# Performance work log

Hardware: AMD Instinct MI355X
Metric: run time of the kernel (lower is better)

## Reference

```python
import jax, jax.numpy as jnp
import numpy as np

EMB = 1024
HID = 2048
HEADS = 16
CONV = 4


def causal_conv1d(z, w):
    # z: [B, H, T], w: [H, K] depthwise causal conv
    K = w.shape[1]
    T = z.shape[-1]
    zp = jnp.pad(z, ((0, 0), (0, 0), (K - 1, 0)))  # [B, H, T+K-1]
    out = jnp.zeros_like(z)
    for k in range(K):  # tiny fixed loop over taps (K<=4)
        out = out + w[None, :, k, None] * jax.lax.dynamic_slice_in_dim(zp, k, T, axis=2)
    return out


def linear_scan(a, b):
    # h_t = a_t * h_{t-1} + b_t along last axis; associative scan
    def combine(c1, c2):
        a1, b1 = c1
        a2, b2 = c2
        return a1 * a2, a2 * b1 + b2
    _, h = jax.lax.associative_scan(combine, (a, b), axis=-1)
    return h


def setup_inputs() -> dict:
    key = jax.random.key(0)
    k1, k2, k3, k4 = jax.random.split(key, 4)
    x = jax.random.normal(k1, (4, 2048, EMB), dtype=jnp.float32)
    w1 = jax.random.normal(k2, (3 * HID, EMB), dtype=jnp.float32) * (EMB ** -0.5)
    w2 = jax.random.normal(k3, (EMB, HID), dtype=jnp.float32) * (HID ** -0.5)
    conv_weight = jax.random.normal(k4, (HID, CONV), dtype=jnp.float32) * (CONV ** -0.5)
    return {"x": x, "w1": w1, "w2": w2, "conv_weight": conv_weight}


def reference(x, w1, w2, conv_weight):
    bsz, seq_len, _ = x.shape
    head_dim = HID // HEADS
    y = jnp.einsum("bse,he->bsh", x, w1)  # [B, S, 3*HID]
    out1, z, h = jnp.split(y, 3, axis=-1)
    z = jnp.swapaxes(z, 1, 2)  # [B, HID, S]
    h = jnp.swapaxes(h, 1, 2)
    z = causal_conv1d(z, conv_weight)
    z = jax.nn.sigmoid(z)
    z = z.reshape(bsz * HEADS, head_dim, seq_len)
    h = h.reshape(bsz * HEADS, head_dim, seq_len)
    h = linear_scan(1.0 - z, z * h)
    out2 = jnp.swapaxes(h.reshape(bsz, HID, seq_len), 1, 2)  # [B, S, HID]
    out = jax.nn.silu(out1) * out2
    return jnp.einsum("bsh,eh->bse", out, w2)
```

## Files before the change

### kernel.cpp

```cpp
#include <hip/hip_runtime.h>
#include <cstdint>

#define EMB 1024
#define HID 2048
#define BATCH 4
#define SEQ 2048
#define MROWS (BATCH * SEQ)
#define N1 (3 * HID)
#define K1 EMB
#define N2 EMB
#define K2 HID

#define NX (MROWS * EMB)
#define NW1 (N1 * K1)
#define NW2 (N2 * K2)

#define SEG 64
#define SLEN (SEQ / SEG)

typedef unsigned short ushort_t;
typedef __bf16 bf16x8 __attribute__((ext_vector_type(8)));
typedef float f32x4 __attribute__((ext_vector_type(4)));
typedef ushort_t us4 __attribute__((ext_vector_type(4)));

__device__ __forceinline__ ushort_t f2bf(float f) {
    uint32_t u = __builtin_bit_cast(uint32_t, f);
    u += 0x7fffu + ((u >> 16) & 1u);
    return (ushort_t)(u >> 16);
}
__device__ __forceinline__ float bf2f(ushort_t h) {
    uint32_t u = ((uint32_t)h) << 16;
    return __builtin_bit_cast(float, u);
}
__device__ __forceinline__ float bflo(uint32_t v) {
    return __builtin_bit_cast(float, v << 16);
}
__device__ __forceinline__ float bfhi(uint32_t v) {
    return __builtin_bit_cast(float, v & 0xffff0000u);
}
__device__ __forceinline__ float sigm(float x) {
    return 1.f / (1.f + __expf(-x));
}

__device__ __forceinline__ void gload_lds16(const ushort_t* g, const ushort_t* l) {
    __builtin_amdgcn_global_load_lds(
        (const __attribute__((address_space(1))) void*)(uintptr_t)(g),
        (__attribute__((address_space(3))) void*)(uint32_t)(uintptr_t)(l),
        16, 0, 0);
}

__global__ __launch_bounds__(256) void cvt_kernel(
    const float* __restrict__ x, const float* __restrict__ w1,
    const float* __restrict__ w2, ushort_t* __restrict__ xb,
    ushort_t* __restrict__ w1b, ushort_t* __restrict__ w2b) {
    const int i = (blockIdx.x * 256 + threadIdx.x) * 4;
    const float* s;
    ushort_t* d;
    if (i < NX) {
        s = x + i; d = xb + i;
    } else if (i < NX + NW1) {
        s = w1 + (i - NX); d = w1b + (i - NX);
    } else {
        s = w2 + (i - NX - NW1); d = w2b + (i - NX - NW1);
    }
    const float4 v = *(const float4*)s;
    us4 o;
    o.x = f2bf(v.x); o.y = f2bf(v.y); o.z = f2bf(v.z); o.w = f2bf(v.w);
    *(us4*)d = o;
}

template <bool OUT_BF16>
__global__ __launch_bounds__(512, 2) void gemm256(
    const ushort_t* __restrict__ A, const ushort_t* __restrict__ B,
    void* __restrict__ Cv, int M, int N, int K) {
    __shared__ __align__(16) ushort_t sA[4][2][4096];
    __shared__ __align__(16) ushort_t sB[4][2][4096];

    const int tid  = threadIdx.x;
    const int lane = tid & 63;
    const int wave = tid >> 6;
    const int wm   = wave >> 2;
    const int wn   = wave & 3;
    const int quad = lane >> 4;
    const int l15  = lane & 15;

    int wg = blockIdx.x;
    const int nwg = gridDim.x;
    if ((nwg & 7) == 0) wg = (wg & 7) * (nwg >> 3) + (wg >> 3);
    const int nbx = N >> 8;
    const int bx = wg % nbx;
    const int by = wg / nbx;
    const long tm0 = (long)by << 8;
    const long tn0 = (long)bx << 8;

    const ushort_t* gA = A + (size_t)tm0 * K;
    const ushort_t* gB = B + (size_t)tn0 * K;

    const int l8g = lane >> 3;
    const int l7g = lane & 7;
    const int s8  = l7g ^ l8g;
    const int mloc = (l8g << 1) + (s8 >> 2);
    const uint32_t soff = (uint32_t)(wave * 16 + mloc) * (uint32_t)K +
                          (uint32_t)((s8 & 3) << 3);

    const auto STG = [&](int tt) {
        const int ib = tt & 3;
        const size_t ko = (size_t)tt * 32;
        gload_lds16(gA + ko + soff, &sA[ib][0][wave << 9]);
        gload_lds16(gA + ko + (size_t)128 * K + soff, &sA[ib][1][wave << 9]);
        gload_lds16(gB + ko + soff, &sB[ib][0][wave << 9]);
        gload_lds16(gB + ko + (size_t)128 * K + soff, &sB[ib][1][wave << 9]);
    };

    const int stored = ((((l15 & 1) << 2) + quad) ^ ((l15 >> 1) & 7));
    const int abase  = (l15 >> 1) * 64 + stored * 8;
    const int bbase  = ((wn & 1) << 11) + abase;

    f32x4 acc[8][4] = {};
    bf16x8 aX[8], bX[4], aY[8], bY[4];

    const int NT = K >> 5;

    STG(0); STG(1); STG(2);
    asm volatile("s_waitcnt vmcnt(4)" ::: "memory");
    __builtin_amdgcn_s_barrier();

    {
        const ushort_t* pa = &sA[0][wm][0];
        const ushort_t* pb = &sB[0][wn >> 1][0];
#pragma unroll
        for (int i = 0; i < 8; ++i) aX[i] = *(const bf16x8*)&pa[abase + i * 512];
#pragma unroll
        for (int j = 0; j < 4; ++j) bX[j] = *(const bf16x8*)&pb[bbase + j * 512];
    }

    const auto body = [&](int T, bf16x8 (&ac)[8], bf16x8 (&bc)[4],
                                 bf16x8 (&an)[8], bf16x8 (&bn)[4]) {
        const int ibn = (T + 1) & 3;
        const ushort_t* pa = &sA[ibn][wm][0];
        const ushort_t* pb = &sB[ibn][wn >> 1][0];
        const bool rd = (T + 1 < NT);
        const bool st = (T + 3 < NT);
        if (rd) {
#pragma unroll
            for (int i = 0; i < 4; ++i)
                an[i] = *(const bf16x8*)&pa[abase + i * 512];
        }
        __builtin_amdgcn_s_setprio(1);
#pragma unroll
        for (int i = 0; i < 4; ++i)
#pragma unroll
            for (int j = 0; j < 4; ++j)
                acc[i][j] = __builtin_amdgcn_mfma_f32_16x16x32_bf16(
                    ac[i], bc[j], acc[i][j], 0, 0, 0);
        __builtin_amdgcn_s_setprio(0);
        if (rd) {
#pragma unroll
            for (int i = 4; i < 8; ++i)
                an[i] = *(const bf16x8*)&pa[abase + i * 512];
#pragma unroll
            for (int j = 0; j < 4; ++j)
                bn[j] = *(const bf16x8*)&pb[bbase + j * 512];
        }
        __builtin_amdgcn_s_setprio(1);
#pragma unroll
        for (int i = 4; i < 8; ++i)
#pragma unroll
            for (int j = 0; j < 4; ++j)
                acc[i][j] = __builtin_amdgcn_mfma_f32_16x16x32_bf16(
                    ac[i], bc[j], acc[i][j], 0, 0, 0);
        __builtin_amdgcn_s_setprio(0);
        if (st) {
            STG(T + 3);
            asm volatile("s_waitcnt vmcnt(4)" ::: "memory");
        } else {
            asm volatile("s_waitcnt vmcnt(0)" ::: "memory");
        }
        __builtin_amdgcn_s_barrier();
    };

    for (int T = 0; T < NT; T += 2) {
        body(T, aX, bX, aY, bY);
        body(T + 1, aY, bY, aX, bX);
    }

#pragma unroll
    for (int i = 0; i < 8; ++i) {
        const long row0 = tm0 + wm * 128 + i * 16 + quad * 4;
#pragma unroll
        for (int j = 0; j < 4; ++j) {
            const long col = tn0 + wn * 64 + j * 16 + l15;
#pragma unroll
            for (int r = 0; r < 4; ++r) {
                if constexpr (OUT_BF16) {
                    ((ushort_t*)Cv)[(size_t)(row0 + r) * N + col] = f2bf(acc[i][j][r]);
                } else {
                    ((float*)Cv)[(size_t)(row0 + r) * N + col] = acc[i][j][r];
                }
            }
        }
    }
}

__device__ __forceinline__ void lda4(bf16x8 (&af)[2][4], const ushort_t* c,
                                     int arow, int quad, int sw) {
#pragma unroll
    for (int s = 0; s < 2; ++s)
#pragma unroll
        for (int i = 0; i < 4; ++i)
            af[s][i] = *(const bf16x8*)&c[(arow + i * 16) * 64 +
                                          (((s * 4 + quad) ^ sw) << 3)];
}

__global__ __launch_bounds__(512, 1) void gemm_mn(
    const ushort_t* __restrict__ A, const ushort_t* __restrict__ B,
    float* __restrict__ C, int M, int N, int K) {
    __shared__ __align__(16) ushort_t sA[3][2][8192];
    __shared__ __align__(16) ushort_t sB[3][8192];

    const int tid  = threadIdx.x;
    const int lane = tid & 63;
    const int wave = tid >> 6;
    const int wm   = wave >> 1;
    const int wn   = wave & 1;
    const int quad = lane >> 4;
    const int l15  = lane & 15;
    const int sw   = lane & 7;

    int wg = blockIdx.x;
    const int nwg = gridDim.x;
    if ((nwg & 7) == 0) wg = (wg & 7) * (nwg >> 3) + (wg >> 3);
    const int nbx = N >> 7;
    const int bx = wg % nbx;
    const int by = wg / nbx;
    const long tm0 = (long)by << 8;
    const long tn0 = (long)bx << 7;

    const ushort_t* gA = A + (size_t)tm0 * K;
    const ushort_t* gB = B + (size_t)tn0 * K;

    const int l8 = lane >> 3;
    const int ss = (lane & 7) ^ l8;
    const uint32_t rA = (uint32_t)((wave & 3) * 16 + l8 + (wave >> 2) * 128);
    const uint32_t rB = (uint32_t)(wave * 16 + l8);
    const uint32_t offA0 = rA * (uint32_t)K + (uint32_t)ss * 8u;
    const uint32_t offA1 = offA0 + 8u * (uint32_t)K;
    const uint32_t offB0 = rB * (uint32_t)K + (uint32_t)ss * 8u;
    const uint32_t offB1 = offB0 + 8u * (uint32_t)K;

    const auto stA = [&](int tt, int q) {
        ushort_t* d = &sA[tt % 3][q][wave << 10];
        const size_t ko = (size_t)tt * 64 + (size_t)q * 64 * (size_t)K;
        gload_lds16(gA + ko + offA0, d);
        gload_lds16(gA + ko + offA1, d + 512);
    };
    const auto stB = [&](int tt) {
        ushort_t* d = &sB[tt % 3][wave << 10];
        const size_t ko = (size_t)tt * 64;
        gload_lds16(gB + ko + offB0, d);
        gload_lds16(gB + ko + offB1, d + 512);
    };

    const int cq   = wm & 1;
    const int arow = (wm >> 1) * 64 + l15;
    const int bcol = wn * 64 + l15;

    f32x4 acc[4][4] = {};
    bf16x8 af[2][4], bf[2][4];

    const int NT = K >> 6;

    stA(0, 0); stA(0, 1); stB(0);
    stA(1, 0); stA(1, 1); stB(1);
    asm volatile("s_waitcnt vmcnt(6)" ::: "memory");
    __builtin_amdgcn_s_barrier();

    for (int T = 0; T < NT; ++T) {
        const int cur = T % 3;
        const ushort_t* pa = &sA[cur][cq][0];
        const ushort_t* pb = &sB[cur][0];
        const bool st2 = (T + 2 < NT);

        lda4(af, pa, arow, quad, sw);
        lda4(bf, pb, bcol, quad, sw);
        if (st2) { stA(T + 2, 0); stA(T + 2, 1); stB(T + 2); }
        __builtin_amdgcn_s_setprio(1);
#pragma unroll
        for (int s = 0; s < 2; ++s)
#pragma unroll
            for (int i = 0; i < 4; ++i)
#pragma unroll
                for (int j = 0; j < 4; ++j)
                    acc[i][j] = __builtin_amdgcn_mfma_f32_16x16x32_bf16(
                        af[s][i], bf[s][j], acc[i][j], 0, 0, 0);
        __builtin_amdgcn_s_setprio(0);
        if (st2)                asm volatile("s_waitcnt vmcnt(6)" ::: "memory");
        else if (T + 1 < NT)    asm volatile("s_waitcnt vmcnt(0)" ::: "memory");
        __builtin_amdgcn_s_barrier();
    }

#pragma unroll
    for (int i = 0; i < 4; ++i) {
        const long row0 = tm0 + wm * 64 + i * 16 + quad * 4;
#pragma unroll
        for (int j = 0; j < 4; ++j) {
            const long col = tn0 + wn * 64 + j * 16 + l15;
#pragma unroll
            for (int r = 0; r < 4; ++r)
                C[(size_t)(row0 + r) * N + col] = acc[i][j][r];
        }
    }
}

__global__ __launch_bounds__(256) void scan_part1(
    const ushort_t* __restrict__ y, const float* __restrict__ cw,
    float* __restrict__ Ag, float* __restrict__ Bg) {
    const int gid = blockIdx.x * 256 + threadIdx.x;
    const int ch  = (gid & 1023) * 2;
    const int bs  = gid >> 10;
    const int b   = bs >> 6;
    const int seg = bs & 63;
    const int t0  = seg * SLEN;
    const size_t rowbase = (size_t)b * SEQ;
    const ushort_t* yz = y + 2048 + ch;
    const ushort_t* yh = y + 4096 + ch;

    float w[2][4];
#pragma unroll
    for (int c = 0; c < 2; ++c)
#pragma unroll
        for (int k = 0; k < 4; ++k) w[c][k] = cw[(ch + c) * 4 + k];

    auto ld2 = [&](const ushort_t* p, int t) -> uint32_t {
        return *(const uint32_t*)(p + (rowbase + (size_t)t) * 6144);
    };
    auto zpair = [&](int t, float* out) {
        if (t < 0) { out[0] = 0.f; out[1] = 0.f; }
        else { uint32_t v = ld2(yz, t); out[0] = bflo(v); out[1] = bfhi(v); }
    };

    float z1[2], z2[2], z3[2], A[2] = {1.f, 1.f}, Bv[2] = {0.f, 0.f};
    zpair(t0 - 1, z1); zpair(t0 - 2, z2); zpair(t0 - 3, z3);

#pragma unroll 8
    for (int t = t0; t < t0 + SLEN; ++t) {
        const uint32_t vz = ld2(yz, t);
        const uint32_t vh = ld2(yh, t);
        const float zr[2] = {bflo(vz), bfhi(vz)};
        const float hr[2] = {bflo(vh), bfhi(vh)};
#pragma unroll
        for (int c = 0; c < 2; ++c) {
            const float cv = w[c][0] * z3[c] + w[c][1] * z2[c] +
                             w[c][2] * z1[c] + w[c][3] * zr[c];
            const float s = sigm(cv);
            z3[c] = z2[c]; z2[c] = z1[c]; z1[c] = zr[c];
            const float a = 1.f - s;
            A[c] *= a;
            Bv[c] = a * Bv[c] + s * hr[c];
        }
    }
    const size_t idx = ((size_t)b * SEG + seg) * HID + ch;
    *(float2*)&Ag[idx] = make_float2(A[0], A[1]);
    *(float2*)&Bg[idx] = make_float2(Bv[0], Bv[1]);
}

__global__ __launch_bounds__(256) void scan_part2(
    const float* __restrict__ Ag, const float* __restrict__ Bg,
    float* __restrict__ Cr) {
    const int gid = blockIdx.x * 256 + threadIdx.x;
    const int b  = gid >> 11;
    const int ch = gid & 2047;
    float carry = 0.f;
#pragma unroll
    for (int s = 0; s < SEG; ++s) {
        const size_t idx = ((size_t)b * SEG + s) * HID + ch;
        Cr[idx] = carry;
        carry = Ag[idx] * carry + Bg[idx];
    }
}

__global__ __launch_bounds__(256) void scan_part3(
    const ushort_t* __restrict__ y, const float* __restrict__ cw,
    const float* __restrict__ Cr, ushort_t* __restrict__ u) {
    const int gid = blockIdx.x * 256 + threadIdx.x;
    const int ch  = (gid & 1023) * 2;
    const int bs  = gid >> 10;
    const int b   = bs >> 6;
    const int seg = bs & 63;
    const int t0  = seg * SLEN;
    const size_t rowbase = (size_t)b * SEQ;
    const ushort_t* yo = y + ch;
    const ushort_t* yz = y + 2048 + ch;
    const ushort_t* yh = y + 4096 + ch;

    float w[2][4];
#pragma unroll
    for (int c = 0; c < 2; ++c)
#pragma unroll
        for (int k = 0; k < 4; ++k) w[c][k] = cw[(ch + c) * 4 + k];

    auto ld2 = [&](const ushort_t* p, int t) -> uint32_t {
        return *(const uint32_t*)(p + (rowbase + (size_t)t) * 6144);
    };
    auto zpair = [&](int t, float* out) {
        if (t < 0) { out[0] = 0.f; out[1] = 0.f; }
        else { uint32_t v = ld2(yz, t); out[0] = bflo(v); out[1] = bfhi(v); }
    };

    const size_t cidx = ((size_t)b * SEG + seg) * HID + ch;
    float h[2] = {Cr[cidx], Cr[cidx + 1]};
    float z1[2], z2[2], z3[2];
    zpair(t0 - 1, z1); zpair(t0 - 2, z2); zpair(t0 - 3, z3);

#pragma unroll 8
    for (int t = t0; t < t0 + SLEN; ++t) {
        const uint32_t vz = ld2(yz, t);
        const uint32_t vh = ld2(yh, t);
        const uint32_t vo = ld2(yo, t);
        const float zr[2] = {bflo(vz), bfhi(vz)};
        const float hr[2] = {bflo(vh), bfhi(vh)};
        const float o1[2] = {bflo(vo), bfhi(vo)};
        ushort_t res[2];
#pragma unroll
        for (int c = 0; c < 2; ++c) {
            const float cv = w[c][0] * z3[c] + w[c][1] * z2[c] +
                             w[c][2] * z1[c] + w[c][3] * zr[c];
            const float s = sigm(cv);
            z3[c] = z2[c]; z2[c] = z1[c]; z1[c] = zr[c];
            h[c] = (1.f - s) * h[c] + s * hr[c];
            const float sil = o1[c] * sigm(o1[c]);
            res[c] = f2bf(sil * h[c]);
        }
        *(uint32_t*)&u[(rowbase + (size_t)t) * (size_t)HID + ch] =
            (uint32_t)res[0] | ((uint32_t)res[1] << 16);
    }
}

extern "C" void kernel_launch(void* const* d_in, const int* in_sizes, int n_in,
                              void* d_out, int out_size, void* d_ws, size_t ws_size,
                              hipStream_t stream) {
    const float* x  = (const float*)d_in[0];
    const float* w1 = (const float*)d_in[1];
    const float* w2 = (const float*)d_in[2];
    const float* cw = (const float*)d_in[3];
    char* ws = (char*)d_ws;

    ushort_t* xb  = (ushort_t*)(ws);
    ushort_t* w1b = (ushort_t*)(ws + (size_t)16777216);
    ushort_t* w2b = (ushort_t*)(ws + (size_t)29360128);
    ushort_t* y   = (ushort_t*)(ws + (size_t)33554432);
    ushort_t* u   = (ushort_t*)(ws + (size_t)134217728);
    float* Ag = (float*)(ws);
    float* Bg = (float*)(ws + (size_t)2097152);
    float* Cr = (float*)(ws + (size_t)4194304);
    float* out = (float*)d_out;

    cvt_kernel<<<16384, 256, 0, stream>>>(x, w1, w2, xb, w1b, w2b);
    gemm256<true><<<dim3(768), 512, 0, stream>>>(xb, w1b, (void*)y, MROWS, N1, K1);
    scan_part1<<<1024, 256, 0, stream>>>(y, cw, Ag, Bg);
    scan_part2<<<32, 256, 0, stream>>>(Ag, Bg, Cr);
    scan_part3<<<1024, 256, 0, stream>>>(y, cw, Cr, u);
    gemm_mn<<<dim3(256), 512, 0, stream>>>(u, w2b, out, MROWS, N2, K2);
}
```

Baseline: 295.5 us.

## Unify both GEMMs into one register-double-buffered, deeper-prefetch 256x128 kernel

Replaces the 256x256-tile first GEMM with the 256x128-tile kernel previously used only for the second GEMM, now templated on output type. That kernel gains register double-buffering of LDS fragments and a third global-to-LDS stage in flight, with an extra barrier per iteration. The goal is to hide LDS-read latency behind MFMA work and to give the first GEMM more workgroups. In exchange, the first GEMM loses operand reuse from its larger tile and pays for a second barrier per step. The LDS footprint likely prevents the requested two blocks per CU.

```diff
diff --git a/kernel.cpp b/kernel.cpp
--- a/kernel.cpp
+++ b/kernel.cpp
@@ -69,139 +69,6 @@
     *(us4*)d = o;
 }
 
-template <bool OUT_BF16>
-__global__ __launch_bounds__(512, 2) void gemm256(
-    const ushort_t* __restrict__ A, const ushort_t* __restrict__ B,
-    void* __restrict__ Cv, int M, int N, int K) {
-    __shared__ __align__(16) ushort_t sA[4][2][4096];
-    __shared__ __align__(16) ushort_t sB[4][2][4096];
-
-    const int tid  = threadIdx.x;
-    const int lane = tid & 63;
-    const int wave = tid >> 6;
-    const int wm   = wave >> 2;
-    const int wn   = wave & 3;
-    const int quad = lane >> 4;
-    const int l15  = lane & 15;
-
-    int wg = blockIdx.x;
-    const int nwg = gridDim.x;
-    if ((nwg & 7) == 0) wg = (wg & 7) * (nwg >> 3) + (wg >> 3);
-    const int nbx = N >> 8;
-    const int bx = wg % nbx;
-    const int by = wg / nbx;
-    const long tm0 = (long)by << 8;
-    const long tn0 = (long)bx << 8;
-
-    const ushort_t* gA = A + (size_t)tm0 * K;
-    const ushort_t* gB = B + (size_t)tn0 * K;
-
-    const int l8g = lane >> 3;
-    const int l7g = lane & 7;
-    const int s8  = l7g ^ l8g;
-    const int mloc = (l8g << 1) + (s8 >> 2);
-    const uint32_t soff = (uint32_t)(wave * 16 + mloc) * (uint32_t)K +
-                          (uint32_t)((s8 & 3) << 3);
-
-    const auto STG = [&](int tt) {
-        const int ib = tt & 3;
-        const size_t ko = (size_t)tt * 32;
-        gload_lds16(gA + ko + soff, &sA[ib][0][wave << 9]);
-        gload_lds16(gA + ko + (size_t)128 * K + soff, &sA[ib][1][wave << 9]);
-        gload_lds16(gB + ko + soff, &sB[ib][0][wave << 9]);
-        gload_lds16(gB + ko + (size_t)128 * K + soff, &sB[ib][1][wave << 9]);
-    };
-
-    const int stored = ((((l15 & 1) << 2) + quad) ^ ((l15 >> 1) & 7));
-    const int abase  = (l15 >> 1) * 64 + stored * 8;
-    const int bbase  = ((wn & 1) << 11) + abase;
-
-    f32x4 acc[8][4] = {};
-    bf16x8 aX[8], bX[4], aY[8], bY[4];
-
-    const int NT = K >> 5;
-
-    STG(0); STG(1); STG(2);
-    asm volatile("s_waitcnt vmcnt(4)" ::: "memory");
-    __builtin_amdgcn_s_barrier();
-
-    {
-        const ushort_t* pa = &sA[0][wm][0];
-        const ushort_t* pb = &sB[0][wn >> 1][0];
-#pragma unroll
-        for (int i = 0; i < 8; ++i) aX[i] = *(const bf16x8*)&pa[abase + i * 512];
-#pragma unroll
-        for (int j = 0; j < 4; ++j) bX[j] = *(const bf16x8*)&pb[bbase + j * 512];
-    }
-
-    const auto body = [&](int T, bf16x8 (&ac)[8], bf16x8 (&bc)[4],
-                                 bf16x8 (&an)[8], bf16x8 (&bn)[4]) {
-        const int ibn = (T + 1) & 3;
-        const ushort_t* pa = &sA[ibn][wm][0];
-        const ushort_t* pb = &sB[ibn][wn >> 1][0];
-        const bool rd = (T + 1 < NT);
-        const bool st = (T + 3 < NT);
-        if (rd) {
-#pragma unroll
-            for (int i = 0; i < 4; ++i)
-                an[i] = *(const bf16x8*)&pa[abase + i * 512];
-        }
-        __builtin_amdgcn_s_setprio(1);
-#pragma unroll
-        for (int i = 0; i < 4; ++i)
-#pragma unroll
-            for (int j = 0; j < 4; ++j)
-                acc[i][j] = __builtin_amdgcn_mfma_f32_16x16x32_bf16(
-                    ac[i], bc[j], acc[i][j], 0, 0, 0);
-        __builtin_amdgcn_s_setprio(0);
-        if (rd) {
-#pragma unroll
-            for (int i = 4; i < 8; ++i)
-                an[i] = *(const bf16x8*)&pa[abase + i * 512];
-#pragma unroll
-            for (int j = 0; j < 4; ++j)
-                bn[j] = *(const bf16x8*)&pb[bbase + j * 512];
-        }
-        __builtin_amdgcn_s_setprio(1);
-#pragma unroll
-        for (int i = 4; i < 8; ++i)
-#pragma unroll
-            for (int j = 0; j < 4; ++j)
-                acc[i][j] = __builtin_amdgcn_mfma_f32_16x16x32_bf16(
-                    ac[i], bc[j], acc[i][j], 0, 0, 0);
-        __builtin_amdgcn_s_setprio(0);
-        if (st) {
-            STG(T + 3);
-            asm volatile("s_waitcnt vmcnt(4)" ::: "memory");
-        } else {
-            asm volatile("s_waitcnt vmcnt(0)" ::: "memory");
-        }
-        __builtin_amdgcn_s_barrier();
-    };
-
-    for (int T = 0; T < NT; T += 2) {
-        body(T, aX, bX, aY, bY);
-        body(T + 1, aY, bY, aX, bX);
-    }
-
-#pragma unroll
-    for (int i = 0; i < 8; ++i) {
-        const long row0 = tm0 + wm * 128 + i * 16 + quad * 4;
-#pragma unroll
-        for (int j = 0; j < 4; ++j) {
-            const long col = tn0 + wn * 64 + j * 16 + l15;
-#pragma unroll
-            for (int r = 0; r < 4; ++r) {
-                if constexpr (OUT_BF16) {
-                    ((ushort_t*)Cv)[(size_t)(row0 + r) * N + col] = f2bf(acc[i][j][r]);
-                } else {
-                    ((float*)Cv)[(size_t)(row0 + r) * N + col] = acc[i][j][r];
-                }
-            }
-        }
-    }
-}
-
 __device__ __forceinline__ void lda4(bf16x8 (&af)[2][4], const ushort_t* c,
                                      int arow, int quad, int sw) {
 #pragma unroll
@@ -212,9 +79,10 @@
                                           (((s * 4 + quad) ^ sw) << 3)];
 }
 
-__global__ __launch_bounds__(512, 1) void gemm_mn(
+template <bool OUT_BF16>
+__global__ __launch_bounds__(512, 2) void gemm_p(
     const ushort_t* __restrict__ A, const ushort_t* __restrict__ B,
-    float* __restrict__ C, int M, int N, int K) {
+    void* __restrict__ Cv, int M, int N, int K) {
     __shared__ __align__(16) ushort_t sA[3][2][8192];
     __shared__ __align__(16) ushort_t sB[3][8192];
 
@@ -266,24 +134,25 @@
     const int bcol = wn * 64 + l15;
 
     f32x4 acc[4][4] = {};
-    bf16x8 af[2][4], bf[2][4];
+    bf16x8 afX[2][4], bfX[2][4], afY[2][4], bfY[2][4];
 
     const int NT = K >> 6;
 
     stA(0, 0); stA(0, 1); stB(0);
     stA(1, 0); stA(1, 1); stB(1);
+    stA(2, 0); stA(2, 1); stB(2);
     asm volatile("s_waitcnt vmcnt(6)" ::: "memory");
     __builtin_amdgcn_s_barrier();
-
-    for (int T = 0; T < NT; ++T) {
-        const int cur = T % 3;
-        const ushort_t* pa = &sA[cur][cq][0];
-        const ushort_t* pb = &sB[cur][0];
-        const bool st2 = (T + 2 < NT);
-
-        lda4(af, pa, arow, quad, sw);
-        lda4(bf, pb, bcol, quad, sw);
-        if (st2) { stA(T + 2, 0); stA(T + 2, 1); stB(T + 2); }
+    lda4(afX, &sA[0][cq][0], arow, quad, sw);
+    lda4(bfX, &sB[0][0],     bcol, quad, sw);
+
+    const auto body = [&](int T, bf16x8 (&ca)[2][4], bf16x8 (&cb)[2][4],
+                                 bf16x8 (&na)[2][4], bf16x8 (&nb)[2][4]) {
+        if (T + 1 < NT) {
+            const int ib = (T + 1) % 3;
+            lda4(na, &sA[ib][cq][0], arow, quad, sw);
+            lda4(nb, &sB[ib][0],     bcol, quad, sw);
+        }
         __builtin_amdgcn_s_setprio(1);
 #pragma unroll
         for (int s = 0; s < 2; ++s)
@@ -292,11 +161,21 @@
 #pragma unroll
                 for (int j = 0; j < 4; ++j)
                     acc[i][j] = __builtin_amdgcn_mfma_f32_16x16x32_bf16(
-                        af[s][i], bf[s][j], acc[i][j], 0, 0, 0);
+                        ca[s][i], cb[s][j], acc[i][j], 0, 0, 0);
         __builtin_amdgcn_s_setprio(0);
-        if (st2)                asm volatile("s_waitcnt vmcnt(6)" ::: "memory");
-        else if (T + 1 < NT)    asm volatile("s_waitcnt vmcnt(0)" ::: "memory");
         __builtin_amdgcn_s_barrier();
+        if (T + 3 < NT) {
+            stA(T + 3, 0); stA(T + 3, 1); stB(T + 3);
+            asm volatile("s_waitcnt vmcnt(6)" ::: "memory");
+        } else {
+            asm volatile("s_waitcnt vmcnt(0)" ::: "memory");
+        }
+        __builtin_amdgcn_s_barrier();
+    };
+
+    for (int T = 0; T < NT; T += 2) {
+        body(T,     afX, bfX, afY, bfY);
+        body(T + 1, afY, bfY, afX, bfX);
     }
 
 #pragma unroll
@@ -306,8 +185,13 @@
         for (int j = 0; j < 4; ++j) {
             const long col = tn0 + wn * 64 + j * 16 + l15;
 #pragma unroll
-            for (int r = 0; r < 4; ++r)
-                C[(size_t)(row0 + r) * N + col] = acc[i][j][r];
+            for (int r = 0; r < 4; ++r) {
+                if constexpr (OUT_BF16) {
+                    ((ushort_t*)Cv)[(size_t)(row0 + r) * N + col] = f2bf(acc[i][j][r]);
+                } else {
+                    ((float*)Cv)[(size_t)(row0 + r) * N + col] = acc[i][j][r];
+                }
+            }
         }
     }
 }
@@ -456,9 +340,9 @@
     float* out = (float*)d_out;
 
     cvt_kernel<<<16384, 256, 0, stream>>>(x, w1, w2, xb, w1b, w2b);
-    gemm256<true><<<dim3(768), 512, 0, stream>>>(xb, w1b, (void*)y, MROWS, N1, K1);
+    gemm_p<true><<<dim3(1536), 512, 0, stream>>>(xb, w1b, (void*)y, MROWS, N1, K1);
     scan_part1<<<1024, 256, 0, stream>>>(y, cw, Ag, Bg);
     scan_part2<<<32, 256, 0, stream>>>(Ag, Bg, Cr);
     scan_part3<<<1024, 256, 0, stream>>>(y, cw, Cr, u);
-    gemm_mn<<<dim3(256), 512, 0, stream>>>(u, w2b, out, MROWS, N2, K2);
-}
+    gemm_p<false><<<dim3(256), 512, 0, stream>>>(u, w2b, (void*)out, MROWS, N2, K2);
+}
```

Result: slower. 343.6 us (+16.3%).
